# Kernel tuning notes

Hardware: AMD Instinct MI355X
Metric: run time of the kernel (lower is better)

Reference implementation:

```python
import jax, jax.numpy as jnp
import numpy as np

GATE_CAP = 15.0
NH = 8
DH = 128  # head_dim = embedding_dim // num_heads
EPS_BACKEND = 1e-6
EPS_NORM = 1e-6


def soft_cap(z, cap):
    return cap * jnp.tanh(z / cap)


def setup_inputs() -> dict:
    key = jax.random.key(0)
    ks = jax.random.split(key, 9)
    B, S, D = 2, 2048, 1024
    s = lambda n: (1.0 / np.sqrt(n)).astype(np.float32) if isinstance(n, np.ndarray) else np.float32(1.0 / np.sqrt(n))
    return {
        "x": jax.random.normal(ks[0], (B, S, D), jnp.float32),
        "Wq": jax.random.normal(ks[1], (D, D), jnp.float32) * s(D),
        "Wk": jax.random.normal(ks[2], (DH, D), jnp.float32) * s(D),
        "Wv": jax.random.normal(ks[3], (DH, D), jnp.float32) * s(D),
        "Wog": jax.random.normal(ks[4], (D, D), jnp.float32) * s(D),
        "Wi": jax.random.normal(ks[5], (NH, D), jnp.float32) * s(D),
        "bi": jnp.zeros((NH,), jnp.float32),
        "Wf": jax.random.normal(ks[6], (NH, D), jnp.float32) * s(D),
        "bf": jnp.ones((NH,), jnp.float32),
        "ln_w": jnp.ones((D,), jnp.float32),
        "Wout": jax.random.normal(ks[7], (D, D), jnp.float32) * s(D),
    }


def reference(x, Wq, Wk, Wv, Wog, Wi, bi, Wf, bf, ln_w, Wout):
    B, S, D = x.shape
    # projections (single weight mode, use_bias=False except gates)
    q = jnp.einsum("bsd,ed->bse", x, Wq).reshape(B, S, NH, DH).transpose(0, 2, 1, 3)  # [B,NH,S,DH]
    k = jnp.einsum("bsd,ed->bse", x, Wk)[:, None, :, :]  # [B,1,S,DH] (num_key_value_heads=1)
    v = jnp.einsum("bsd,ed->bse", x, Wv)[:, None, :, :]
    k = jnp.broadcast_to(k, (B, NH, S, DH))  # repeat_kv
    v = jnp.broadcast_to(v, (B, NH, S, DH))
    o_preact = jnp.einsum("bsd,ed->bse", x, Wog)  # [B,S,D]
    i_pre = soft_cap(jnp.einsum("bsd,hd->bhs", x, Wi) + bi[None, :, None], GATE_CAP)  # [B,NH,S]
    f_pre = soft_cap(jnp.einsum("bsd,hd->bhs", x, Wf) + bf[None, :, None], GATE_CAP)

    # native parallel mLSTM backend (stabilized), no initial state
    log_f = jax.nn.log_sigmoid(f_pre)               # [B,NH,S]
    csum = jnp.cumsum(log_f, axis=-1)
    mat_log_f = csum[:, :, :, None] - csum[:, :, None, :]  # [B,NH,S,S]
    ltr = jnp.tril(jnp.ones((S, S), dtype=bool))
    mat_log_f = jnp.where(ltr, mat_log_f, -jnp.inf)
    mat_log_d = mat_log_f + i_pre[:, :, None, :]
    vec_m = jnp.max(mat_log_d, axis=-1, keepdims=True)      # [B,NH,S,1]
    mat_d = jnp.exp(mat_log_d - vec_m)
    mat_s = jnp.einsum("bhsd,bhtd->bhst", q, k) * (DH ** -0.5)
    mat_c = mat_s * mat_d
    vec_n = jnp.maximum(jnp.abs(jnp.sum(mat_c, axis=-1, keepdims=True)), jnp.exp(-vec_m))
    C = mat_c / (vec_n + EPS_BACKEND)
    h = jnp.einsum("bhst,bhtd->bhsd", C, v)  # [B,NH,S,DH]

    # multihead layernorm (per-head, fp32 reductions, weight only)
    h = h.transpose(0, 2, 1, 3)  # [B,S,NH,DH]
    h32 = h.astype(jnp.float32)
    mu = jnp.mean(h32, axis=-1, keepdims=True)
    var = jnp.mean(jnp.square(h32 - mu), axis=-1, keepdims=True)
    h_norm = ((h32 - mu) * jax.lax.rsqrt(var + EPS_NORM)).astype(h.dtype)
    h_norm = h_norm * ln_w.reshape(NH, DH)[None, None, :, :]
    h_norm = h_norm.reshape(B, S, D)

    h_out = jax.nn.sigmoid(o_preact) * h_norm
    y = jnp.einsum("bsd,ed->bse", h_out, Wout)
    return y
```

## Files before the change

### kernel.cpp

```cpp
#include <hip/hip_runtime.h>


typedef __bf16 bf16x8 __attribute__((ext_vector_type(8)));
typedef float f32x4 __attribute__((ext_vector_type(4)));
typedef unsigned short us8 __attribute__((ext_vector_type(8)));
typedef unsigned short us4 __attribute__((ext_vector_type(4)));

__device__ __forceinline__ unsigned short f2bf(float f) {
    unsigned int u = __builtin_bit_cast(unsigned int, f);
    unsigned int r = u + 0x7fffu + ((u >> 16) & 1u);
    return (unsigned short)(r >> 16);
}
__device__ __forceinline__ float bf2f(unsigned short h) {
    unsigned int u = ((unsigned int)h) << 16;
    return __builtin_bit_cast(float, u);
}
__device__ __forceinline__ f32x4 mfma16(bf16x8 a, bf16x8 b, f32x4 c) {
    return __builtin_amdgcn_mfma_f32_16x16x32_bf16(a, b, c, 0, 0, 0);
}

__global__ __launch_bounds__(256) void k_split_bf16(const float* __restrict__ in,
                                                    unsigned short* __restrict__ hi,
                                                    unsigned short* __restrict__ lo, int n) {
    int i = blockIdx.x * 256 + threadIdx.x;
    if (i < n) {
        float f = in[i];
        unsigned short h = f2bf(f);
        hi[i] = h;
        lo[i] = f2bf(f - bf2f(h));
    }
}

__global__ __launch_bounds__(256) void build_wcat(const float* __restrict__ Wq,
                                                  const float* __restrict__ Wk,
                                                  const float* __restrict__ Wv,
                                                  const float* __restrict__ Wog,
                                                  unsigned short* __restrict__ wh,
                                                  unsigned short* __restrict__ wl) {
    int idx = blockIdx.x * 256 + threadIdx.x;
    if (idx >= 2304 * 1024) return;
    int row = idx >> 10, col = idx & 1023;
    float v;
    if (row < 1024)      v = Wq[(size_t)row * 1024 + col] * 0.08838834764831845f;
    else if (row < 1152) v = Wk[(size_t)(row - 1024) * 1024 + col];
    else if (row < 1280) v = Wv[(size_t)(row - 1152) * 1024 + col];
    else                 v = Wog[(size_t)(row - 1280) * 1024 + col];
    unsigned short h = f2bf(v);
    wh[idx] = h;
    wl[idx] = f2bf(v - bf2f(h));
}

__global__ __launch_bounds__(256) void gates_kernel(const float* __restrict__ x,
                                                    const float* __restrict__ Wi,
                                                    const float* __restrict__ bi,
                                                    const float* __restrict__ Wf,
                                                    const float* __restrict__ bfb,
                                                    float* __restrict__ ipre,
                                                    float* __restrict__ lgf) {
    int bs = blockIdx.x;
    int b = bs >> 11, s = bs & 2047;
    const float* xr = x + (size_t)bs * 1024;
    int lane = threadIdx.x & 63, w = threadIdx.x >> 6;
    const float* W = (w < 2) ? Wi : Wf;
    int h0 = (w & 1) * 4;
    float dot0 = 0.f, dot1 = 0.f, dot2 = 0.f, dot3 = 0.f;
    for (int i = lane; i < 1024; i += 64) {
        float xv = xr[i];
        dot0 += xv * W[(size_t)(h0 + 0) * 1024 + i];
        dot1 += xv * W[(size_t)(h0 + 1) * 1024 + i];
        dot2 += xv * W[(size_t)(h0 + 2) * 1024 + i];
        dot3 += xv * W[(size_t)(h0 + 3) * 1024 + i];
    }
#pragma unroll
    for (int o = 32; o; o >>= 1) {
        dot0 += __shfl_xor(dot0, o);
        dot1 += __shfl_xor(dot1, o);
        dot2 += __shfl_xor(dot2, o);
        dot3 += __shfl_xor(dot3, o);
    }
    if (lane == 0) {
        float d[4] = {dot0, dot1, dot2, dot3};
#pragma unroll
        for (int j = 0; j < 4; j++) {
            int hh = h0 + j;
            if (w < 2) {
                float z = d[j] + bi[hh];
                z = 15.f * tanhf(z * (1.f / 15.f));
                ipre[((size_t)b * 8 + hh) * 2048 + s] = z;
            } else {
                float z = d[j] + bfb[hh];
                z = 15.f * tanhf(z * (1.f / 15.f));
                lgf[((size_t)b * 8 + hh) * 2048 + s] = fminf(z, 0.f) - log1pf(expf(-fabsf(z)));
            }
        }
    }
}

__global__ void scan_kernel(const float* __restrict__ ipre, const float* __restrict__ lgf,
                            float* __restrict__ csum, float* __restrict__ aarr,
                            float* __restrict__ marr) {
    int bh = blockIdx.x;
    int lane = threadIdx.x;
    const float* lf = lgf + (size_t)bh * 2048;
    const float* ip = ipre + (size_t)bh * 2048;
    float* cs = csum + (size_t)bh * 2048;
    float* aa = aarr + (size_t)bh * 2048;
    float* mm = marr + (size_t)bh * 2048;
    float carry = 0.f;
    float carrym = -1e30f;
    for (int c = 0; c < 32; c++) {
        float v = lf[c * 64 + lane];
#pragma unroll
        for (int o = 1; o < 64; o <<= 1) {
            float t = __shfl_up(v, o);
            if (lane >= o) v += t;
        }
        float cval = carry + v;
        cs[c * 64 + lane] = cval;
        float a = ip[c * 64 + lane] - cval;
        aa[c * 64 + lane] = a;
        float mv = a;
#pragma unroll
        for (int o = 1; o < 64; o <<= 1) {
            float t = __shfl_up(mv, o);
            if (lane >= o) mv = fmaxf(mv, t);
        }
        float mval = fmaxf(carrym, mv);
        mm[c * 64 + lane] = mval;
        carry = __shfl(cval, 63);
        carrym = __shfl(mval, 63);
    }
}

__global__ __launch_bounds__(256) void gemm_bt3(const unsigned short* __restrict__ Ah,
                                                const unsigned short* __restrict__ Al,
                                                const unsigned short* __restrict__ Bh,
                                                const unsigned short* __restrict__ Bl,
                                                void* __restrict__ Cp,
                                                unsigned short* __restrict__ Clo,
                                                int K, int ldc, int c_bf16, int og_y0) {
    __shared__ __attribute__((aligned(16))) unsigned short Ash[128 * 40];
    __shared__ __attribute__((aligned(16))) unsigned short Asl[128 * 40];
    __shared__ __attribute__((aligned(16))) unsigned short Bsh[128 * 40];
    __shared__ __attribute__((aligned(16))) unsigned short Bsl[128 * 40];
    const int tid = threadIdx.x;
    const int lane = tid & 63, wv = tid >> 6;
    const int wr = wv >> 1, wc = wv & 1;
    const int fr = lane & 15, fg = lane >> 4;
    const int srow = tid >> 1, scol = (tid & 1) * 16;
    const bool full3 = (blockIdx.y < (unsigned)og_y0);
    const size_t aoff = (size_t)(blockIdx.x * 128 + srow) * K + scol;
    const size_t boff = (size_t)(blockIdx.y * 128 + srow) * K + scol;
    f32x4 acc[4][4] = {};
    for (int kt = 0; kt < K; kt += 32) {
        us8 avh0 = *(const us8*)(Ah + aoff + kt);
        us8 avh1 = *(const us8*)(Ah + aoff + kt + 8);
        us8 avl0 = *(const us8*)(Al + aoff + kt);
        us8 avl1 = *(const us8*)(Al + aoff + kt + 8);
        us8 bvh0 = *(const us8*)(Bh + boff + kt);
        us8 bvh1 = *(const us8*)(Bh + boff + kt + 8);
        us8 bvl0 = *(const us8*)(Bl + boff + kt);
        us8 bvl1 = *(const us8*)(Bl + boff + kt + 8);
        __syncthreads();
        *(us8*)&Ash[srow * 40 + scol] = avh0;
        *(us8*)&Ash[srow * 40 + scol + 8] = avh1;
        *(us8*)&Asl[srow * 40 + scol] = avl0;
        *(us8*)&Asl[srow * 40 + scol + 8] = avl1;
        *(us8*)&Bsh[srow * 40 + scol] = bvh0;
        *(us8*)&Bsh[srow * 40 + scol + 8] = bvh1;
        *(us8*)&Bsl[srow * 40 + scol] = bvl0;
        *(us8*)&Bsl[srow * 40 + scol + 8] = bvl1;
        __syncthreads();
        bf16x8 bfh[4], bfl[4];
#pragma unroll
        for (int j = 0; j < 4; j++) {
            bfh[j] = __builtin_bit_cast(bf16x8, *(const us8*)&Bsh[(64 * wc + 16 * j + fr) * 40 + fg * 8]);
            bfl[j] = __builtin_bit_cast(bf16x8, *(const us8*)&Bsl[(64 * wc + 16 * j + fr) * 40 + fg * 8]);
        }
        __builtin_amdgcn_s_setprio(1);
        if (full3) {
#pragma unroll
            for (int i = 0; i < 4; i++) {
                bf16x8 afh = __builtin_bit_cast(bf16x8, *(const us8*)&Ash[(64 * wr + 16 * i + fr) * 40 + fg * 8]);
                bf16x8 afl = __builtin_bit_cast(bf16x8, *(const us8*)&Asl[(64 * wr + 16 * i + fr) * 40 + fg * 8]);
#pragma unroll
                for (int j = 0; j < 4; j++) {
                    acc[i][j] = mfma16(afh, bfh[j], acc[i][j]);
                    acc[i][j] = mfma16(afh, bfl[j], acc[i][j]);
                    acc[i][j] = mfma16(afl, bfh[j], acc[i][j]);
                }
            }
        } else {
#pragma unroll
            for (int i = 0; i < 4; i++) {
                bf16x8 afh = __builtin_bit_cast(bf16x8, *(const us8*)&Ash[(64 * wr + 16 * i + fr) * 40 + fg * 8]);
#pragma unroll
                for (int j = 0; j < 4; j++)
                    acc[i][j] = mfma16(afh, bfh[j], acc[i][j]);
            }
        }
        __builtin_amdgcn_s_setprio(0);
    }
#pragma unroll
    for (int i = 0; i < 4; i++)
#pragma unroll
        for (int j = 0; j < 4; j++)
#pragma unroll
            for (int e = 0; e < 4; e++) {
                int r = blockIdx.x * 128 + 64 * wr + 16 * i + fg * 4 + e;
                int c = blockIdx.y * 128 + 64 * wc + 16 * j + fr;
                float v = acc[i][j][e];
                if (c_bf16) {
                    unsigned short h = f2bf(v);
                    ((unsigned short*)Cp)[(size_t)r * ldc + c] = h;
                    Clo[(size_t)r * ldc + c] = f2bf(v - bf2f(h));
                } else {
                    ((float*)Cp)[(size_t)r * ldc + c] = v;
                }
            }
}

__global__ __launch_bounds__(256) void make_vt(const unsigned short* __restrict__ ph,
                                               const unsigned short* __restrict__ pl,
                                               unsigned short* __restrict__ vTh,
                                               unsigned short* __restrict__ vTl) {
    __shared__ __attribute__((aligned(16))) unsigned short th[64 * 68];
    __shared__ __attribute__((aligned(16))) unsigned short tl[64 * 68];
    const int bid = blockIdx.x;
    const int st = bid & 31, ct = (bid >> 5) & 1, b = bid >> 6;
    const int tid = threadIdx.x;
    {
        const int sr = tid >> 2, cc = (tid & 3) * 16;
        const size_t rbase = (size_t)(b * 2048 + st * 64 + sr) * 2304 + 1152 + ct * 64 + cc;
        us8 a0 = *(const us8*)(ph + rbase);
        us8 a1 = *(const us8*)(ph + rbase + 8);
        us8 c0 = *(const us8*)(pl + rbase);
        us8 c1 = *(const us8*)(pl + rbase + 8);
        *(us8*)&th[sr * 68 + cc] = a0;
        *(us8*)&th[sr * 68 + cc + 8] = a1;
        *(us8*)&tl[sr * 68 + cc] = c0;
        *(us8*)&tl[sr * 68 + cc + 8] = c1;
    }
    __syncthreads();
    {
        const int cr = tid >> 2, ss = (tid & 3) * 16;
        us8 oh0, oh1, ol0, ol1;
#pragma unroll
        for (int e = 0; e < 8; e++) {
            oh0[e] = th[(ss + e) * 68 + cr];
            oh1[e] = th[(ss + 8 + e) * 68 + cr];
            ol0[e] = tl[(ss + e) * 68 + cr];
            ol1[e] = tl[(ss + 8 + e) * 68 + cr];
        }
        const size_t wbase = (size_t)b * 128 * 2048 + (size_t)(ct * 64 + cr) * 2048 + st * 64 + ss;
        *(us8*)&vTh[wbase] = oh0;
        *(us8*)&vTh[wbase + 8] = oh1;
        *(us8*)&vTl[wbase] = ol0;
        *(us8*)&vTl[wbase + 8] = ol1;
    }
}

__global__ __launch_bounds__(256, 2) void attn_fused(const unsigned short* __restrict__ projh,
                                                     const unsigned short* __restrict__ projl,
                                                     const unsigned short* __restrict__ vTh,
                                                     const unsigned short* __restrict__ vTl,
                                                     const float* __restrict__ aarr,
                                                     const float* __restrict__ marr,
                                                     const float* __restrict__ csum,
                                                     const float* __restrict__ lnw,
                                                     unsigned short* __restrict__ ho_hi,
                                                     unsigned short* __restrict__ ho_lo) {
    __shared__ __attribute__((aligned(16))) unsigned short Klh[2][32 * 148];
    __shared__ __attribute__((aligned(16))) unsigned short Kll[2][32 * 148];
    __shared__ __attribute__((aligned(16))) unsigned short Vlh[2][128 * 40];
    __shared__ __attribute__((aligned(16))) unsigned short Vll[2][128 * 40];
    __shared__ float al[2][32];

    const int idx = blockIdx.x;
    const int half = idx >> 8;
    const int pid = idx & 255;
    const int bh = pid & 15;
    const int qt0 = pid >> 4;
    const int qt = half ? (31 - qt0) : qt0;
    const int b = bh >> 3, h = bh & 7;
    const int tid = threadIdx.x, lane = tid & 63, w = tid >> 6;
    const int fr = lane & 15, fg = lane >> 4;
    const int q0 = qt * 64;
    const int qg = q0 + 16 * w + fr;

    bf16x8 qfh[4], qfl[4];
    {
        const size_t qoff = (size_t)(b * 2048 + qg) * 2304 + h * 128;
#pragma unroll
        for (int ks = 0; ks < 4; ks++) {
            qfh[ks] = __builtin_bit_cast(bf16x8, *(const us8*)(projh + qoff + ks * 32 + fg * 8));
            qfl[ks] = __builtin_bit_cast(bf16x8, *(const us8*)(projl + qoff + ks * 32 + fg * 8));
        }
    }
    const float ma_q = marr[(size_t)bh * 2048 + qg];

    f32x4 acc[8] = {};
    float b_run = 0.f;

    const int kr = tid >> 3, kc = (tid & 7) * 16;
    const int vr = tid >> 1, vc = (tid & 1) * 16;
    const size_t kbase = (size_t)(b * 2048) * 2304 + 1024;
    const size_t vtbase = (size_t)b * 128 * 2048;

    const int nt = 2 * qt + 2;
    us8 kh0, kh1, kl0, kl1, vh0, vh1, vl0, vl1;
    float a_st;
#define LOADT(T0)                                                              \
    {                                                                          \
        const size_t ko = kbase + (size_t)((T0) + kr) * 2304 + kc;             \
        const size_t vo = vtbase + (size_t)vr * 2048 + (T0) + vc;              \
        kh0 = *(const us8*)(projh + ko);                                       \
        kh1 = *(const us8*)(projh + ko + 8);                                   \
        kl0 = *(const us8*)(projl + ko);                                       \
        kl1 = *(const us8*)(projl + ko + 8);                                   \
        vh0 = *(const us8*)(vTh + vo);                                         \
        vh1 = *(const us8*)(vTh + vo + 8);                                     \
        vl0 = *(const us8*)(vTl + vo);                                         \
        vl1 = *(const us8*)(vTl + vo + 8);                                     \
        a_st = (tid < 32) ? aarr[(size_t)bh * 2048 + (T0) + tid] : 0.f;        \
    }
#define STORET(BUF)                                                            \
    {                                                                          \
        *(us8*)&Klh[BUF][kr * 148 + kc] = kh0;                                 \
        *(us8*)&Klh[BUF][kr * 148 + kc + 8] = kh1;                             \
        *(us8*)&Kll[BUF][kr * 148 + kc] = kl0;                                 \
        *(us8*)&Kll[BUF][kr * 148 + kc + 8] = kl1;                             \
        *(us8*)&Vlh[BUF][vr * 40 + vc] = vh0;                                  \
        *(us8*)&Vlh[BUF][vr * 40 + vc + 8] = vh1;                              \
        *(us8*)&Vll[BUF][vr * 40 + vc] = vl0;                                  \
        *(us8*)&Vll[BUF][vr * 40 + vc + 8] = vl1;                              \
        if (tid < 32) al[BUF][tid] = a_st;                                     \
    }

    LOADT(0);
    STORET(0);
    if (nt > 1) LOADT(32);
    __syncthreads();

    for (int kt = 0; kt < nt; kt++) {
        const int cur = kt & 1;
        const int t0 = kt * 32;
        if (kt + 1 < nt) {
            STORET(cur ^ 1);
            if (kt + 2 < nt) LOADT((kt + 2) * 32);
        }

        float dj[2][4];
#pragma unroll
        for (int j = 0; j < 2; j++) {
            f32x4 sfa = {}, sfb = {}, sfc = {};
            __builtin_amdgcn_s_setprio(1);
#pragma unroll
            for (int ks = 0; ks < 4; ks++) {
                bf16x8 kfh = __builtin_bit_cast(bf16x8, *(const us8*)&Klh[cur][(j * 16 + fr) * 148 + ks * 32 + fg * 8]);
                bf16x8 kfl = __builtin_bit_cast(bf16x8, *(const us8*)&Kll[cur][(j * 16 + fr) * 148 + ks * 32 + fg * 8]);
                sfa = mfma16(kfh, qfh[ks], sfa);
                sfb = mfma16(kfh, qfl[ks], sfb);
                sfc = mfma16(kfl, qfh[ks], sfc);
            }
            __builtin_amdgcn_s_setprio(0);
            f32x4 sf = (sfa + sfb) + sfc;
#pragma unroll
            for (int r = 0; r < 4; r++) {
                const int kloc = j * 16 + fg * 4 + r;
                const int key = t0 + kloc;
                const float atv = al[cur][kloc];
                dj[j][r] = (key <= qg) ? sf[r] * __expf(atv - ma_q) : 0.f;
            }
        }

        {
            float ts = dj[0][0] + dj[0][1] + dj[0][2] + dj[0][3]
                     + dj[1][0] + dj[1][1] + dj[1][2] + dj[1][3];
            ts += __shfl_xor(ts, 16);
            ts += __shfl_xor(ts, 32);
            b_run += ts;
        }

        float p8[8];
        const int srlo = 32 * ((lane >> 4) & 1) + fr;
#pragma unroll
        for (int e = 0; e < 8; e++) {
            const int sl = srlo + ((e >= 4) ? 16 : 0);
            const float v0 = __shfl(dj[0][e & 3], sl);
            const float v1 = __shfl(dj[1][e & 3], sl);
            p8[e] = (lane & 32) ? v1 : v0;
        }
        us8 phu, plu;
#pragma unroll
        for (int e = 0; e < 8; e++) {
            unsigned short hh = f2bf(p8[e]);
            phu[e] = hh;
            plu[e] = f2bf(p8[e] - bf2f(hh));
        }
        const bf16x8 pfh = __builtin_bit_cast(bf16x8, phu);
        const bf16x8 pfl = __builtin_bit_cast(bf16x8, plu);

        __builtin_amdgcn_s_setprio(1);
#pragma unroll
        for (int jb = 0; jb < 8; jb++) {
            bf16x8 vfh = __builtin_bit_cast(bf16x8, *(const us8*)&Vlh[cur][(jb * 16 + fr) * 40 + fg * 8]);
            bf16x8 vfl = __builtin_bit_cast(bf16x8, *(const us8*)&Vll[cur][(jb * 16 + fr) * 40 + fg * 8]);
            acc[jb] = mfma16(vfh, pfh, acc[jb]);
            acc[jb] = mfma16(vfh, pfl, acc[jb]);
            acc[jb] = mfma16(vfl, pfh, acc[jb]);
        }
        __builtin_amdgcn_s_setprio(0);
        __syncthreads();
    }
#undef LOADT
#undef STORET

    const float cs_q = csum[(size_t)bh * 2048 + qg];
    const float nf = __expf(-(cs_q + ma_q));
    const float n = fmaxf(fabsf(b_run), nf);
    const float inv = 1.f / (n + 1e-6f);
#pragma unroll
    for (int jb = 0; jb < 8; jb++) acc[jb] *= inv;

    float s1 = 0.f;
#pragma unroll
    for (int jb = 0; jb < 8; jb++) s1 += acc[jb][0] + acc[jb][1] + acc[jb][2] + acc[jb][3];
    s1 += __shfl_xor(s1, 16);
    s1 += __shfl_xor(s1, 32);
    const float mu = s1 * (1.f / 128.f);
    float vv = 0.f;
#pragma unroll
    for (int jb = 0; jb < 8; jb++)
#pragma unroll
        for (int e = 0; e < 4; e++) {
            float d = acc[jb][e] - mu;
            vv += d * d;
        }
    vv += __shfl_xor(vv, 16);
    vv += __shfl_xor(vv, 32);
    const float rstd = rsqrtf(vv * (1.f / 128.f) + 1e-6f);

    const size_t obase = (size_t)(b * 2048 + qg) * 2304 + 1280 + h * 128 + fg * 4;
    const size_t hbase = (size_t)(b * 2048 + qg) * 1024 + h * 128 + fg * 4;
#pragma unroll
    for (int jb = 0; jb < 8; jb++) {
        us4 ogh = *(const us4*)(projh + obase + jb * 16);
        us4 ogl = *(const us4*)(projl + obase + jb * 16);
        f32x4 lw = *(const f32x4*)&lnw[h * 128 + jb * 16 + fg * 4];
        us4 hi4, lo4;
#pragma unroll
        for (int e = 0; e < 4; e++) {
            const float og = bf2f(ogh[e]) + bf2f(ogl[e]);
            const float sig = 1.f / (1.f + __expf(-og));
            const float ho = (acc[jb][e] - mu) * rstd * lw[e] * sig;
            unsigned short h1 = f2bf(ho);
            hi4[e] = h1;
            lo4[e] = f2bf(ho - bf2f(h1));
        }
        *(us4*)&ho_hi[hbase + jb * 16] = hi4;
        *(us4*)&ho_lo[hbase + jb * 16] = lo4;
    }
}

extern "C" void kernel_launch(void* const* d_in, const int* in_sizes, int n_in,
                              void* d_out, int out_size, void* d_ws, size_t ws_size,
                              hipStream_t stream) {
    (void)in_sizes; (void)n_in; (void)out_size; (void)ws_size;
    const float* x    = (const float*)d_in[0];
    const float* Wq   = (const float*)d_in[1];
    const float* Wk   = (const float*)d_in[2];
    const float* Wv   = (const float*)d_in[3];
    const float* Wog  = (const float*)d_in[4];
    const float* Wi   = (const float*)d_in[5];
    const float* bi   = (const float*)d_in[6];
    const float* Wf   = (const float*)d_in[7];
    const float* bfb  = (const float*)d_in[8];
    const float* lnw  = (const float*)d_in[9];
    const float* Wout = (const float*)d_in[10];

    char* p = (char*)d_ws;
    auto carve = [&](size_t bytes) -> char* {
        char* r = p;
        p += (bytes + 255) & ~(size_t)255;
        return r;
    };
    unsigned short* x_hi   = (unsigned short*)carve(4194304ull * 2);
    unsigned short* x_lo   = (unsigned short*)carve(4194304ull * 2);
    unsigned short* wc_hi  = (unsigned short*)carve(2359296ull * 2);
    unsigned short* wc_lo  = (unsigned short*)carve(2359296ull * 2);
    unsigned short* wo_hi  = (unsigned short*)carve(1048576ull * 2);
    unsigned short* wo_lo  = (unsigned short*)carve(1048576ull * 2);
    unsigned short* pr_hi  = (unsigned short*)carve(4096ull * 2304 * 2);
    unsigned short* pr_lo  = (unsigned short*)carve(4096ull * 2304 * 2);
    unsigned short* vT_hi  = (unsigned short*)carve(524288ull * 2);
    unsigned short* vT_lo  = (unsigned short*)carve(524288ull * 2);
    float* ipre    = (float*)carve(32768ull * 4);
    float* lgf_buf = (float*)carve(32768ull * 4);
    float* csum    = (float*)carve(32768ull * 4);
    float* aarr    = (float*)carve(32768ull * 4);
    float* marr    = (float*)carve(32768ull * 4);
    unsigned short* ho_hi = x_hi;
    unsigned short* ho_lo = x_lo;

    k_split_bf16<<<16384, 256, 0, stream>>>(x, x_hi, x_lo, 4194304);
    build_wcat<<<(2359296 + 255) / 256, 256, 0, stream>>>(Wq, Wk, Wv, Wog, wc_hi, wc_lo);
    k_split_bf16<<<4096, 256, 0, stream>>>(Wout, wo_hi, wo_lo, 1048576);
    gates_kernel<<<4096, 256, 0, stream>>>(x, Wi, bi, Wf, bfb, ipre, lgf_buf);
    scan_kernel<<<16, 64, 0, stream>>>(ipre, lgf_buf, csum, aarr, marr);
    gemm_bt3<<<dim3(32, 18), 256, 0, stream>>>(x_hi, x_lo, wc_hi, wc_lo, pr_hi, pr_lo, 1024, 2304, 1, 10);
    make_vt<<<128, 256, 0, stream>>>(pr_hi, pr_lo, vT_hi, vT_lo);
    attn_fused<<<512, 256, 0, stream>>>(pr_hi, pr_lo, vT_hi, vT_lo, aarr, marr, csum, lnw, ho_hi, ho_lo);
    gemm_bt3<<<dim3(32, 8), 256, 0, stream>>>(ho_hi, ho_lo, wo_hi, wo_lo, d_out, nullptr, 1024, 1024, 0, 1000);
}
```

Baseline: 339.5 us.

## Process two key tiles per iteration in mLSTM attention loop

Restructures the attention inner loop to handle two 32-key tiles per iteration: both LDS buffers hold the current pair, and the next pair is prefetched into registers. The QK MFMAs of the two tiles are interleaved so independent chains can overlap, and barrier count per key drops. The cost is double the prefetch registers, which may hurt occupancy. LDS is no longer double-buffered across iterations, so two barriers now wrap each store phase.

```diff
diff --git a/kernel.cpp b/kernel.cpp
--- a/kernel.cpp
+++ b/kernel.cpp
@@ -308,113 +308,180 @@
     const size_t vtbase = (size_t)b * 128 * 2048;
 
     const int nt = 2 * qt + 2;
-    us8 kh0, kh1, kl0, kl1, vh0, vh1, vl0, vl1;
-    float a_st;
-#define LOADT(T0)                                                              \
+    us8 kh0A, kh1A, kl0A, kl1A, vh0A, vh1A, vl0A, vl1A;
+    us8 kh0B, kh1B, kl0B, kl1B, vh0B, vh1B, vl0B, vl1B;
+    float a_stA, a_stB;
+#define LOADPAIR(T0)                                                           \
     {                                                                          \
-        const size_t ko = kbase + (size_t)((T0) + kr) * 2304 + kc;             \
-        const size_t vo = vtbase + (size_t)vr * 2048 + (T0) + vc;              \
-        kh0 = *(const us8*)(projh + ko);                                       \
-        kh1 = *(const us8*)(projh + ko + 8);                                   \
-        kl0 = *(const us8*)(projl + ko);                                       \
-        kl1 = *(const us8*)(projl + ko + 8);                                   \
-        vh0 = *(const us8*)(vTh + vo);                                         \
-        vh1 = *(const us8*)(vTh + vo + 8);                                     \
-        vl0 = *(const us8*)(vTl + vo);                                         \
-        vl1 = *(const us8*)(vTl + vo + 8);                                     \
-        a_st = (tid < 32) ? aarr[(size_t)bh * 2048 + (T0) + tid] : 0.f;        \
-    }
-#define STORET(BUF)                                                            \
+        const size_t koA = kbase + (size_t)((T0) + kr) * 2304 + kc;            \
+        const size_t voA = vtbase + (size_t)vr * 2048 + (T0) + vc;             \
+        kh0A = *(const us8*)(projh + koA);                                     \
+        kh1A = *(const us8*)(projh + koA + 8);                                 \
+        kl0A = *(const us8*)(projl + koA);                                     \
+        kl1A = *(const us8*)(projl + koA + 8);                                 \
+        vh0A = *(const us8*)(vTh + voA);                                       \
+        vh1A = *(const us8*)(vTh + voA + 8);                                   \
+        vl0A = *(const us8*)(vTl + voA);                                       \
+        vl1A = *(const us8*)(vTl + voA + 8);                                   \
+        a_stA = (tid < 32) ? aarr[(size_t)bh * 2048 + (T0) + tid] : 0.f;       \
+        const size_t koB = koA + 32ull * 2304;                                 \
+        const size_t voB = voA + 32;                                           \
+        kh0B = *(const us8*)(projh + koB);                                     \
+        kh1B = *(const us8*)(projh + koB + 8);                                 \
+        kl0B = *(const us8*)(projl + koB);                                     \
+        kl1B = *(const us8*)(projl + koB + 8);                                 \
+        vh0B = *(const us8*)(vTh + voB);                                       \
+        vh1B = *(const us8*)(vTh + voB + 8);                                   \
+        vl0B = *(const us8*)(vTl + voB);                                       \
+        vl1B = *(const us8*)(vTl + voB + 8);                                   \
+        a_stB = (tid < 32) ? aarr[(size_t)bh * 2048 + (T0) + 32 + tid] : 0.f;  \
+    }
+#define STOREPAIR()                                                            \
     {                                                                          \
-        *(us8*)&Klh[BUF][kr * 148 + kc] = kh0;                                 \
-        *(us8*)&Klh[BUF][kr * 148 + kc + 8] = kh1;                             \
-        *(us8*)&Kll[BUF][kr * 148 + kc] = kl0;                                 \
-        *(us8*)&Kll[BUF][kr * 148 + kc + 8] = kl1;                             \
-        *(us8*)&Vlh[BUF][vr * 40 + vc] = vh0;                                  \
-        *(us8*)&Vlh[BUF][vr * 40 + vc + 8] = vh1;                              \
-        *(us8*)&Vll[BUF][vr * 40 + vc] = vl0;                                  \
-        *(us8*)&Vll[BUF][vr * 40 + vc + 8] = vl1;                              \
-        if (tid < 32) al[BUF][tid] = a_st;                                     \
-    }
-
-    LOADT(0);
-    STORET(0);
-    if (nt > 1) LOADT(32);
+        *(us8*)&Klh[0][kr * 148 + kc] = kh0A;                                  \
+        *(us8*)&Klh[0][kr * 148 + kc + 8] = kh1A;                              \
+        *(us8*)&Kll[0][kr * 148 + kc] = kl0A;                                  \
+        *(us8*)&Kll[0][kr * 148 + kc + 8] = kl1A;                              \
+        *(us8*)&Vlh[0][vr * 40 + vc] = vh0A;                                   \
+        *(us8*)&Vlh[0][vr * 40 + vc + 8] = vh1A;                               \
+        *(us8*)&Vll[0][vr * 40 + vc] = vl0A;                                   \
+        *(us8*)&Vll[0][vr * 40 + vc + 8] = vl1A;                               \
+        *(us8*)&Klh[1][kr * 148 + kc] = kh0B;                                  \
+        *(us8*)&Klh[1][kr * 148 + kc + 8] = kh1B;                              \
+        *(us8*)&Kll[1][kr * 148 + kc] = kl0B;                                  \
+        *(us8*)&Kll[1][kr * 148 + kc + 8] = kl1B;                              \
+        *(us8*)&Vlh[1][vr * 40 + vc] = vh0B;                                   \
+        *(us8*)&Vlh[1][vr * 40 + vc + 8] = vh1B;                               \
+        *(us8*)&Vll[1][vr * 40 + vc] = vl0B;                                   \
+        *(us8*)&Vll[1][vr * 40 + vc + 8] = vl1B;                               \
+        if (tid < 32) {                                                        \
+            al[0][tid] = a_stA;                                                \
+            al[1][tid] = a_stB;                                                \
+        }                                                                      \
+    }
+
+    LOADPAIR(0);
+    STOREPAIR();
+    if (nt > 2) LOADPAIR(64);
     __syncthreads();
 
-    for (int kt = 0; kt < nt; kt++) {
-        const int cur = kt & 1;
+    for (int kt = 0;;) {
         const int t0 = kt * 32;
-        if (kt + 1 < nt) {
-            STORET(cur ^ 1);
-            if (kt + 2 < nt) LOADT((kt + 2) * 32);
-        }
-
-        float dj[2][4];
+
+        float djA[2][4], djB[2][4];
 #pragma unroll
         for (int j = 0; j < 2; j++) {
-            f32x4 sfa = {}, sfb = {}, sfc = {};
+            f32x4 sfaA = {}, sfbA = {}, sfcA = {};
+            f32x4 sfaB = {}, sfbB = {}, sfcB = {};
             __builtin_amdgcn_s_setprio(1);
 #pragma unroll
             for (int ks = 0; ks < 4; ks++) {
-                bf16x8 kfh = __builtin_bit_cast(bf16x8, *(const us8*)&Klh[cur][(j * 16 + fr) * 148 + ks * 32 + fg * 8]);
-                bf16x8 kfl = __builtin_bit_cast(bf16x8, *(const us8*)&Kll[cur][(j * 16 + fr) * 148 + ks * 32 + fg * 8]);
-                sfa = mfma16(kfh, qfh[ks], sfa);
-                sfb = mfma16(kfh, qfl[ks], sfb);
-                sfc = mfma16(kfl, qfh[ks], sfc);
+                bf16x8 kfhA = __builtin_bit_cast(bf16x8, *(const us8*)&Klh[0][(j * 16 + fr) * 148 + ks * 32 + fg * 8]);
+                bf16x8 kflA = __builtin_bit_cast(bf16x8, *(const us8*)&Kll[0][(j * 16 + fr) * 148 + ks * 32 + fg * 8]);
+                bf16x8 kfhB = __builtin_bit_cast(bf16x8, *(const us8*)&Klh[1][(j * 16 + fr) * 148 + ks * 32 + fg * 8]);
+                bf16x8 kflB = __builtin_bit_cast(bf16x8, *(const us8*)&Kll[1][(j * 16 + fr) * 148 + ks * 32 + fg * 8]);
+                sfaA = mfma16(kfhA, qfh[ks], sfaA);
+                sfaB = mfma16(kfhB, qfh[ks], sfaB);
+                sfbA = mfma16(kfhA, qfl[ks], sfbA);
+                sfbB = mfma16(kfhB, qfl[ks], sfbB);
+                sfcA = mfma16(kflA, qfh[ks], sfcA);
+                sfcB = mfma16(kflB, qfh[ks], sfcB);
             }
             __builtin_amdgcn_s_setprio(0);
-            f32x4 sf = (sfa + sfb) + sfc;
+            f32x4 sfA = (sfaA + sfbA) + sfcA;
+            f32x4 sfB = (sfaB + sfbB) + sfcB;
 #pragma unroll
             for (int r = 0; r < 4; r++) {
                 const int kloc = j * 16 + fg * 4 + r;
-                const int key = t0 + kloc;
-                const float atv = al[cur][kloc];
-                dj[j][r] = (key <= qg) ? sf[r] * __expf(atv - ma_q) : 0.f;
+                const float atvA = al[0][kloc];
+                const float atvB = al[1][kloc];
+                djA[j][r] = ((t0 + kloc) <= qg) ? sfA[r] * __expf(atvA - ma_q) : 0.f;
+                djB[j][r] = ((t0 + 32 + kloc) <= qg) ? sfB[r] * __expf(atvB - ma_q) : 0.f;
             }
         }
 
         {
-            float ts = dj[0][0] + dj[0][1] + dj[0][2] + dj[0][3]
-                     + dj[1][0] + dj[1][1] + dj[1][2] + dj[1][3];
-            ts += __shfl_xor(ts, 16);
-            ts += __shfl_xor(ts, 32);
-            b_run += ts;
-        }
-
-        float p8[8];
+            float tsA = djA[0][0] + djA[0][1] + djA[0][2] + djA[0][3]
+                      + djA[1][0] + djA[1][1] + djA[1][2] + djA[1][3];
+            tsA += __shfl_xor(tsA, 16);
+            tsA += __shfl_xor(tsA, 32);
+            b_run += tsA;
+            float tsB = djB[0][0] + djB[0][1] + djB[0][2] + djB[0][3]
+                      + djB[1][0] + djB[1][1] + djB[1][2] + djB[1][3];
+            tsB += __shfl_xor(tsB, 16);
+            tsB += __shfl_xor(tsB, 32);
+            b_run += tsB;
+        }
+
         const int srlo = 32 * ((lane >> 4) & 1) + fr;
-#pragma unroll
-        for (int e = 0; e < 8; e++) {
-            const int sl = srlo + ((e >= 4) ? 16 : 0);
-            const float v0 = __shfl(dj[0][e & 3], sl);
-            const float v1 = __shfl(dj[1][e & 3], sl);
-            p8[e] = (lane & 32) ? v1 : v0;
-        }
-        us8 phu, plu;
-#pragma unroll
-        for (int e = 0; e < 8; e++) {
-            unsigned short hh = f2bf(p8[e]);
-            phu[e] = hh;
-            plu[e] = f2bf(p8[e] - bf2f(hh));
-        }
-        const bf16x8 pfh = __builtin_bit_cast(bf16x8, phu);
-        const bf16x8 pfl = __builtin_bit_cast(bf16x8, plu);
-
-        __builtin_amdgcn_s_setprio(1);
-#pragma unroll
-        for (int jb = 0; jb < 8; jb++) {
-            bf16x8 vfh = __builtin_bit_cast(bf16x8, *(const us8*)&Vlh[cur][(jb * 16 + fr) * 40 + fg * 8]);
-            bf16x8 vfl = __builtin_bit_cast(bf16x8, *(const us8*)&Vll[cur][(jb * 16 + fr) * 40 + fg * 8]);
-            acc[jb] = mfma16(vfh, pfh, acc[jb]);
-            acc[jb] = mfma16(vfh, pfl, acc[jb]);
-            acc[jb] = mfma16(vfl, pfh, acc[jb]);
-        }
-        __builtin_amdgcn_s_setprio(0);
+        {
+            float p8[8];
+#pragma unroll
+            for (int e = 0; e < 8; e++) {
+                const int sl = srlo + ((e >= 4) ? 16 : 0);
+                const float v0 = __shfl(djA[0][e & 3], sl);
+                const float v1 = __shfl(djA[1][e & 3], sl);
+                p8[e] = (lane & 32) ? v1 : v0;
+            }
+            us8 phu, plu;
+#pragma unroll
+            for (int e = 0; e < 8; e++) {
+                unsigned short hh = f2bf(p8[e]);
+                phu[e] = hh;
+                plu[e] = f2bf(p8[e] - bf2f(hh));
+            }
+            const bf16x8 pfh = __builtin_bit_cast(bf16x8, phu);
+            const bf16x8 pfl = __builtin_bit_cast(bf16x8, plu);
+            __builtin_amdgcn_s_setprio(1);
+#pragma unroll
+            for (int jb = 0; jb < 8; jb++) {
+                bf16x8 vfh = __builtin_bit_cast(bf16x8, *(const us8*)&Vlh[0][(jb * 16 + fr) * 40 + fg * 8]);
+                bf16x8 vfl = __builtin_bit_cast(bf16x8, *(const us8*)&Vll[0][(jb * 16 + fr) * 40 + fg * 8]);
+                acc[jb] = mfma16(vfh, pfh, acc[jb]);
+                acc[jb] = mfma16(vfh, pfl, acc[jb]);
+                acc[jb] = mfma16(vfl, pfh, acc[jb]);
+            }
+            __builtin_amdgcn_s_setprio(0);
+        }
+        {
+            float p8[8];
+#pragma unroll
+            for (int e = 0; e < 8; e++) {
+                const int sl = srlo + ((e >= 4) ? 16 : 0);
+                const float v0 = __shfl(djB[0][e & 3], sl);
+                const float v1 = __shfl(djB[1][e & 3], sl);
+                p8[e] = (lane & 32) ? v1 : v0;
+            }
+            us8 phu, plu;
+#pragma unroll
+            for (int e = 0; e < 8; e++) {
+                unsigned short hh = f2bf(p8[e]);
+                phu[e] = hh;
+                plu[e] = f2bf(p8[e] - bf2f(hh));
+            }
+            const bf16x8 pfh = __builtin_bit_cast(bf16x8, phu);
+            const bf16x8 pfl = __builtin_bit_cast(bf16x8, plu);
+            __builtin_amdgcn_s_setprio(1);
+#pragma unroll
+            for (int jb = 0; jb < 8; jb++) {
+                bf16x8 vfh = __builtin_bit_cast(bf16x8, *(const us8*)&Vlh[1][(jb * 16 + fr) * 40 + fg * 8]);
+                bf16x8 vfl = __builtin_bit_cast(bf16x8, *(const us8*)&Vll[1][(jb * 16 + fr) * 40 + fg * 8]);
+                acc[jb] = mfma16(vfh, pfh, acc[jb]);
+                acc[jb] = mfma16(vfh, pfl, acc[jb]);
+                acc[jb] = mfma16(vfl, pfh, acc[jb]);
+            }
+            __builtin_amdgcn_s_setprio(0);
+        }
+
+        kt += 2;
+        if (kt >= nt) break;
         __syncthreads();
-    }
-#undef LOADT
-#undef STORET
+        STOREPAIR();
+        if (kt + 2 < nt) LOADPAIR((kt + 2) * 32);
+        __syncthreads();
+    }
+#undef LOADPAIR
+#undef STOREPAIR
 
     const float cs_q = csum[(size_t)bh * 2048 + qg];
     const float nf = __expf(-(cs_q + ma_q));
```

New measurement: 330.7 us. 2.6% less time.
